# Kernel tuning notes

Hardware: AMD Instinct MI355X
Metric: run time of the kernel (lower is better)

Reference implementation:

```python
import jax, jax.numpy as jnp
import numpy as np
import math

# dims
B, T, HFEAT, E = 32, 8, 128, 128
NUM_CLS, NUM_GLOBAL = 4, 2
NSP = NUM_CLS + NUM_GLOBAL            # 6 special tokens
SCALES = (1, 4, 8)
WINDOW = 4
NHEAD = 8
DH = E // NHEAD                        # 16
NLAYERS = 2                            # blocks per scale = ceil(6/3)
NS = len(SCALES)
F = 512                                # dim_feedforward
ROPE_BASE = 100000.0
NEG = -1e9


def setup_inputs() -> dict:
    key = jax.random.key(0)
    ks = jax.random.split(key, 16)
    def rn(k, shape, s=0.02):
        return jax.random.normal(k, shape, jnp.float32) * s
    inp = {
        'embeddings': jax.random.normal(ks[0], (B, T, NSP + HFEAT, E), jnp.float32),
        'cls_tokens': rn(ks[1], (NUM_CLS, E)),
        'global_tokens': rn(ks[2], (NUM_GLOBAL, E)),
        'Wq': rn(ks[3], (NS, NLAYERS, E, E)),
        'bq': jnp.zeros((NS, NLAYERS, E), jnp.float32),
        'Wk': rn(ks[4], (NS, NLAYERS, E, E)),
        'bk': jnp.zeros((NS, NLAYERS, E), jnp.float32),
        'Wv': rn(ks[5], (NS, NLAYERS, E, E)),
        'bv': jnp.zeros((NS, NLAYERS, E), jnp.float32),
        'Wo': rn(ks[6], (NS, NLAYERS, E, E)),
        'bo': jnp.zeros((NS, NLAYERS, E), jnp.float32),
        'ln1_g': jnp.ones((NS, NLAYERS, E), jnp.float32),
        'ln1_b': jnp.zeros((NS, NLAYERS, E), jnp.float32),
        'ln2_g': jnp.ones((NS, NLAYERS, E), jnp.float32),
        'ln2_b': jnp.zeros((NS, NLAYERS, E), jnp.float32),
        'W1': rn(ks[7], (NS, NLAYERS, E, F)),
        'b1': jnp.zeros((NS, NLAYERS, F), jnp.float32),
        'W2': rn(ks[8], (NS, NLAYERS, F, E)),
        'b2': jnp.zeros((NS, NLAYERS, E), jnp.float32),
        'out_g': jnp.ones((E,), jnp.float32),
        'out_b': jnp.zeros((E,), jnp.float32),
    }
    return inp


def _layernorm(x, g, b, eps=1e-5):
    mu = x.mean(-1, keepdims=True)
    var = ((x - mu) ** 2).mean(-1, keepdims=True)
    return (x - mu) * jax.lax.rsqrt(var + eps) * g + b


def _rope(x):
    # x: (BT, L, H, DH); rotate-half RoPE over head dim
    L = x.shape[1]
    half = DH // 2
    inv = ROPE_BASE ** (-jnp.arange(half, dtype=jnp.float32) / half)
    ang = jnp.arange(L, dtype=jnp.float32)[:, None] * inv[None, :]   # (L, half)
    cos = jnp.cos(ang)[None, :, None, :]
    sin = jnp.sin(ang)[None, :, None, :]
    x1, x2 = x[..., :half], x[..., half:]
    return jnp.concatenate([x1 * cos - x2 * sin, x1 * sin + x2 * cos], axis=-1)


def _sparse_bias(L):
    # global(first NSP) rows/cols fully connected, others window +-WINDOW, diag allowed
    i = jnp.arange(L)
    allowed = (jnp.abs(i[:, None] - i[None, :]) <= WINDOW) | (i[:, None] < NSP) | (i[None, :] < NSP)
    return jnp.where(allowed, 0.0, NEG).astype(jnp.float32)  # (L, L) additive


def _encoder(x, s, Wq, bq, Wk, bk, Wv, bv, Wo, bo, ln1_g, ln1_b, ln2_g, ln2_b, W1, b1, W2, b2, bias):
    # x: (BT, L, E); pre-norm transformer encoder with RoPE attention
    BT, L, _ = x.shape
    for l in range(NLAYERS):
        h = _layernorm(x, ln1_g[s, l], ln1_b[s, l])
        q = (h @ Wq[s, l] + bq[s, l]).reshape(BT, L, NHEAD, DH)
        k = (h @ Wk[s, l] + bk[s, l]).reshape(BT, L, NHEAD, DH)
        v = (h @ Wv[s, l] + bv[s, l]).reshape(BT, L, NHEAD, DH)
        q, k = _rope(q), _rope(k)
        scores = jnp.einsum('blhd,bmhd->bhlm', q, k) / math.sqrt(DH) + bias[None, None]
        attn = jax.nn.softmax(scores, axis=-1)
        o = jnp.einsum('bhlm,bmhd->blhd', attn, v).reshape(BT, L, E)
        x = x + o @ Wo[s, l] + bo[s, l]
        h2 = _layernorm(x, ln2_g[s, l], ln2_b[s, l])
        x = x + jax.nn.gelu(h2 @ W1[s, l] + b1[s, l]) @ W2[s, l] + b2[s, l]
    return x


def reference(embeddings, cls_tokens, global_tokens, Wq, bq, Wk, bk, Wv, bv, Wo, bo,
              ln1_g, ln1_b, ln2_g, ln2_b, W1, b1, W2, b2, out_g, out_b):
    Bb, Tt, HC, Ee = embeddings.shape
    feats = embeddings[..., NSP:, :]                                 # (B,T,H,E)
    specials = jnp.broadcast_to(
        jnp.concatenate([cls_tokens, global_tokens], axis=0)[None, None],
        (Bb, Tt, NSP, Ee))
    cls_per_scale = []
    for s, g in enumerate(SCALES):
        H = feats.shape[2]
        K = H // g  # H divisible by all scales
        grouped = feats.reshape(Bb, Tt, K, g, Ee).mean(axis=3)       # contiguous mean grouping
        seq = jnp.concatenate([specials, grouped], axis=2)           # (B,T,L,E)
        L = NSP + K
        x = seq.reshape(Bb * Tt, L, Ee)
        bias = _sparse_bias(L)
        out = _encoder(x, s, Wq, bq, Wk, bk, Wv, bv, Wo, bo,
                       ln1_g, ln1_b, ln2_g, ln2_b, W1, b1, W2, b2, bias)
        cls_per_scale.append(out.reshape(Bb, Tt, L, Ee)[..., :NUM_CLS, :])
    cls_out = jnp.stack(cls_per_scale, axis=0).mean(axis=0)          # (B,T,num_cls,E)
    cls_out = _layernorm(cls_out, out_g, out_b)
    return cls_out.reshape(Bb, Tt, NUM_CLS * Ee)
```

## Files before the change

### kernel.cpp

```cpp
#include <hip/hip_runtime.h>
#include <hip/hip_bf16.h>

#define BT     256
#define EDIM   128
#define NSP    6
#define RT     49664
#define O1     34304
#define O2     44032
#define KSTR   20

typedef unsigned short u16;
typedef short s16x8 __attribute__((ext_vector_type(8)));
typedef float f32x4 __attribute__((ext_vector_type(4)));

__device__ __forceinline__ float u2f(u16 u){ union{unsigned i; float f;} v; v.i=((unsigned)u)<<16; return v.f; }
__device__ __forceinline__ u16 f2u(float f){
  union{float f; unsigned i;} v; v.f = f;
  unsigned r = v.i + 0x7FFF + ((v.i >> 16) & 1);
  return (u16)(r >> 16);
}
__device__ __forceinline__ float ldin(const void* p, size_t idx, int flag){
  return flag ? u2f(((const u16*)p)[idx]) : ((const float*)p)[idx];
}
__device__ __forceinline__ void unp8(uint4 v, float* f){
  f[0]=u2f((u16)(v.x)); f[1]=u2f((u16)(v.x>>16));
  f[2]=u2f((u16)(v.y)); f[3]=u2f((u16)(v.y>>16));
  f[4]=u2f((u16)(v.z)); f[5]=u2f((u16)(v.z>>16));
  f[6]=u2f((u16)(v.w)); f[7]=u2f((u16)(v.w>>16));
}

__device__ __forceinline__ void rowinfo(int row, int& s, int& r, int& L, int& g){
  if (row < O1){ s=0; r=row;    L=134; g=1; }
  else if (row < O2){ s=1; r=row-O1; L=38; g=4; }
  else { s=2; r=row-O2; L=22; g=8; }
}

__device__ __forceinline__ float gelu_f(float x){
  float u = x*(1.5957691216f + 0.0713548162f*x*x);
  return x * __builtin_amdgcn_rcpf(1.f + __expf(-u));
}

__global__ void detect_k(const void* ln1g, int* flagp){
  unsigned v = *(const unsigned*)ln1g;
  *flagp = (v == 0x3F803F80u) ? 1 : 0;
}

struct CArg { const void* src; unsigned dstoff; unsigned n; unsigned inblk; unsigned outblk; };
struct CArgs { CArg a[12]; };
__global__ __launch_bounds__(256) void conv_k(CArgs ca, u16* stage, const int* flagp){
  int i = blockIdx.y;
  int flag = *flagp;
  const CArg& c = ca.a[i];
  for (unsigned idx = blockIdx.x*256u + threadIdx.x; idx < c.n; idx += gridDim.x*256u){
    unsigned blk = idx / c.inblk, r = idx % c.inblk;
    float v = flag ? u2f(((const u16*)c.src)[idx]) : ((const float*)c.src)[idx];
    stage[c.dstoff + blk*c.outblk + r] = flag ? ((const u16*)c.src)[idx] : f2u(v);
  }
}

__global__ __launch_bounds__(256) void convw_k(const void* s0, const void* s1, const void* s2,
                                               u16* dst, int K, int N, int Nsrc, const int* flagp)
{
  int flag = *flagp;
  const void* srcs[3] = {s0, s1, s2};
  int total = 6 * K * N;
  for (int idx = blockIdx.x*256 + threadIdx.x; idx < total; idx += gridDim.x*256) {
    int blk = idx / (K*N);
    int rem = idx % (K*N);
    int j = rem & 7;
    int t = rem >> 3;
    int n = t % N;
    int ck = t / N;
    int k = ck*8 + j;
    int w = n / Nsrc;
    int nn = n - w*Nsrc;
    size_t sidx = (size_t)blk*K*Nsrc + (size_t)k*Nsrc + nn;
    dst[idx] = flag ? ((const u16*)srcs[w])[sidx] : f2u(((const float*)srcs[w])[sidx]);
  }
}

__global__ __launch_bounds__(128) void build_k(const void* __restrict__ emb,
                                               const void* __restrict__ cls,
                                               const void* __restrict__ glob,
                                               float* __restrict__ x,
                                               u16* __restrict__ H,
                                               const u16* __restrict__ lnG,
                                               const u16* __restrict__ lnB,
                                               const int* flagp)
{
  __shared__ float red[4];
  int flag = *flagp;
  int row = blockIdx.x, e = threadIdx.x;
  int s, r, L, g; rowinfo(row, s, r, L, g);
  int seq = r / L, pos = r % L;
  float val;
  if (pos < NSP) {
    val = (pos < 4) ? ldin(cls, pos*EDIM + e, flag) : ldin(glob, (pos-4)*EDIM + e, flag);
  } else {
    int k = pos - NSP;
    size_t base = ((size_t)seq*134 + NSP + (size_t)k*g)*EDIM + e;
    float sum = 0.f;
    for (int j = 0; j < g; j++) sum += ldin(emb, base + (size_t)j*EDIM, flag);
    val = sum / (float)g;
  }
  x[(size_t)row*EDIM + e] = val;
  int wid = e >> 6;
  float sum = val, ss = val*val;
  #pragma unroll
  for (int off = 32; off; off >>= 1) { sum += __shfl_xor(sum, off); ss += __shfl_xor(ss, off); }
  if ((e & 63) == 0) { red[wid] = sum; red[2+wid] = ss; }
  __syncthreads();
  float ts = red[0]+red[1], tss = red[2]+red[3];
  float mu = ts * (1.f/128.f);
  float var = tss * (1.f/128.f) - mu*mu;
  float rs = rsqrtf(var + 1e-5f);
  const u16* gp = lnG + s*2*EDIM;
  const u16* bp = lnB + s*2*EDIM;
  H[(size_t)row*EDIM + e] = f2u((val-mu)*rs*u2f(gp[e]) + u2f(bp[e]));
}

template<int EPI>
__global__ __launch_bounds__(256) void gemm64_k(
    const u16* __restrict__ A,
    const u16* __restrict__ Wt, const u16* __restrict__ Bias,
    u16* __restrict__ C, int ldc, int N, int layer,
    float* __restrict__ X, u16* __restrict__ H,
    const u16* __restrict__ lnG, const u16* __restrict__ lnB, int lnidx)
{
  __shared__ u16 As[4][16*136];
  __shared__ u16 Bs[16*128*8];
  const int row0 = blockIdx.x * 64;
  const int n0 = blockIdx.y * 128;
  const int s = row0 < O1 ? 0 : (row0 < O2 ? 1 : 2);
  const u16* Wp = Wt + (size_t)(s*2+layer)*128*N;
  const u16* bp = Bias + (size_t)(s*2+layer)*N + n0;
  const int tid = threadIdx.x;
  const int lane = tid & 63, w = tid >> 6;
  const int g = lane >> 4, l15 = lane & 15;

  #pragma unroll
  for (int i = 0; i < 4; i++) {
    int unit = lane + i*64;
    int r = unit >> 4, kc = unit & 15;
    *(uint4*)&As[w][r*136 + kc*8] = *(const uint4*)(A + (size_t)(row0 + w*16 + r)*128 + kc*8);
  }
  #pragma unroll
  for (int i = 0; i < 8; i++) {
    int u = tid + i*256;
    int kb = u >> 7, nn = u & 127;
    *(uint4*)&Bs[u*8] = *(const uint4*)(Wp + ((size_t)kb*N + n0 + nn)*8);
  }
  __syncthreads();

  f32x4 acc[8];
  #pragma unroll
  for (int nt = 0; nt < 8; nt++) acc[nt] = (f32x4){0.f,0.f,0.f,0.f};
  #pragma unroll
  for (int ks = 0; ks < 4; ks++) {
    int c = ks*4 + g;
    s16x8 af = *(const s16x8*)&As[w][l15*136 + c*8];
    #pragma unroll
    for (int nt = 0; nt < 8; nt++) {
      s16x8 bf = *(const s16x8*)&Bs[(c*128 + nt*16 + l15)*8];
      acc[nt] = __builtin_amdgcn_mfma_f32_16x16x32_bf16(af, bf, acc[nt], 0, 0, 0);
    }
  }

  float bb[8];
  #pragma unroll
  for (int nt = 0; nt < 8; nt++) bb[nt] = u2f(bp[nt*16 + l15]);

  if (EPI == 0) {
    #pragma unroll
    for (int reg = 0; reg < 4; reg++) {
      int row = row0 + w*16 + g*4 + reg;
      #pragma unroll
      for (int nt = 0; nt < 8; nt++)
        C[(size_t)row*ldc + n0 + nt*16 + l15] = f2u(acc[nt][reg] + bb[nt]);
    }
  } else {
    float gam[8], bet[8];
    const u16* gp = lnG + (s*2+lnidx)*EDIM;
    const u16* bpn = lnB + (s*2+lnidx)*EDIM;
    #pragma unroll
    for (int nt = 0; nt < 8; nt++) { gam[nt] = u2f(gp[nt*16+l15]); bet[nt] = u2f(bpn[nt*16+l15]); }
    #pragma unroll
    for (int reg = 0; reg < 4; reg++) {
      int row = row0 + w*16 + g*4 + reg;
      float vals[8], ps = 0.f, pss = 0.f;
      #pragma unroll
      for (int nt = 0; nt < 8; nt++) {
        size_t cidx = (size_t)row*128 + nt*16 + l15;
        float v = acc[nt][reg] + bb[nt] + X[cidx];
        vals[nt] = v; ps += v; pss += v*v;
      }
      #pragma unroll
      for (int off = 1; off < 16; off <<= 1) { ps += __shfl_xor(ps, off); pss += __shfl_xor(pss, off); }
      float mu = ps * (1.f/128.f);
      float var = pss * (1.f/128.f) - mu*mu;
      float rs = rsqrtf(var + 1e-5f);
      #pragma unroll
      for (int nt = 0; nt < 8; nt++) {
        size_t cidx = (size_t)row*128 + nt*16 + l15;
        X[cidx] = vals[nt];
        H[cidx] = f2u((vals[nt]-mu)*rs*gam[nt] + bet[nt]);
      }
    }
  }
}

template<int LNFUSE>
__global__ __launch_bounds__(256) void ffn_k(
    const u16* __restrict__ A,
    const u16* __restrict__ W1t, const u16* __restrict__ B1,
    const u16* __restrict__ W2t, const u16* __restrict__ B2,
    float* __restrict__ X,
    u16* __restrict__ H, const u16* __restrict__ lnG, const u16* __restrict__ lnB,
    int lnidx, int layer)
{
  __shared__ u16 Ts[4][16*40];
  const int row0 = blockIdx.x * 64;
  const int s = row0 < O1 ? 0 : (row0 < O2 ? 1 : 2);
  const u16* W1p = W1t + (size_t)(s*2+layer)*65536;
  const u16* b1p = B1 + (s*2+layer)*512;
  const u16* W2p = W2t + (size_t)(s*2+layer)*65536;
  const u16* b2p = B2 + (s*2+layer)*128;
  const int tid = threadIdx.x;
  const int lane = tid & 63, w = tid >> 6;
  const int g = lane >> 4, l15 = lane & 15;

  s16x8 af[4];
  {
    const u16* arow = A + (size_t)(row0 + w*16 + l15)*128;
    #pragma unroll
    for (int ks = 0; ks < 4; ks++) af[ks] = *(const s16x8*)(arow + (ks*4 + g)*8);
  }

  const u16* w1base = W1p + ((size_t)g*512 + l15)*8;
  const u16* w2base = W2p + ((size_t)g*128 + l15)*8;

  f32x4 acc2[8];
  #pragma unroll
  for (int nt = 0; nt < 8; nt++) acc2[nt] = (f32x4){0.f,0.f,0.f,0.f};

  s16x8 bw1[8];
  #pragma unroll
  for (int ks = 0; ks < 4; ks++) {
    #pragma unroll
    for (int nt = 0; nt < 2; nt++)
      bw1[ks*2+nt] = *(const s16x8*)(w1base + (size_t)(ks*2048 + nt*16)*8);
  }

  for (int f0 = 0; f0 < 512; f0 += 32) {
    s16x8 bw2[8];
    #pragma unroll
    for (int nt = 0; nt < 8; nt++)
      bw2[nt] = *(const s16x8*)(w2base + (size_t)(f0*16 + nt*16)*8);

    f32x4 acc1[2];
    acc1[0] = (f32x4){0.f,0.f,0.f,0.f};
    acc1[1] = (f32x4){0.f,0.f,0.f,0.f};
    #pragma unroll
    for (int ks = 0; ks < 4; ks++) {
      acc1[0] = __builtin_amdgcn_mfma_f32_16x16x32_bf16(af[ks], bw1[ks*2+0], acc1[0], 0, 0, 0);
      acc1[1] = __builtin_amdgcn_mfma_f32_16x16x32_bf16(af[ks], bw1[ks*2+1], acc1[1], 0, 0, 0);
    }

    {
      int fn = (f0 + 32) & 511;
      #pragma unroll
      for (int ks = 0; ks < 4; ks++) {
        #pragma unroll
        for (int nt = 0; nt < 2; nt++)
          bw1[ks*2+nt] = *(const s16x8*)(w1base + (size_t)(ks*2048 + fn + nt*16)*8);
      }
    }

    #pragma unroll
    for (int nt = 0; nt < 2; nt++) {
      float bb1 = u2f(b1p[f0 + nt*16 + l15]);
      #pragma unroll
      for (int reg = 0; reg < 4; reg++)
        Ts[w][(g*4+reg)*40 + nt*16 + l15] = f2u(gelu_f(acc1[nt][reg] + bb1));
    }

    s16x8 af2 = *(const s16x8*)&Ts[w][l15*40 + g*8];
    #pragma unroll
    for (int nt = 0; nt < 8; nt++)
      acc2[nt] = __builtin_amdgcn_mfma_f32_16x16x32_bf16(af2, bw2[nt], acc2[nt], 0, 0, 0);
  }

  float bb2[8];
  #pragma unroll
  for (int nt = 0; nt < 8; nt++) bb2[nt] = u2f(b2p[nt*16 + l15]);

  if (LNFUSE) {
    float gam[8], bet[8];
    const u16* gp = lnG + (s*2+lnidx)*EDIM;
    const u16* bpn = lnB + (s*2+lnidx)*EDIM;
    #pragma unroll
    for (int nt = 0; nt < 8; nt++) { gam[nt] = u2f(gp[nt*16+l15]); bet[nt] = u2f(bpn[nt*16+l15]); }
    #pragma unroll
    for (int reg = 0; reg < 4; reg++) {
      int row = row0 + w*16 + g*4 + reg;
      float vals[8], ps = 0.f, pss = 0.f;
      #pragma unroll
      for (int nt = 0; nt < 8; nt++) {
        size_t cidx = (size_t)row*128 + nt*16 + l15;
        float v = acc2[nt][reg] + bb2[nt] + X[cidx];
        vals[nt] = v; ps += v; pss += v*v;
      }
      #pragma unroll
      for (int off = 1; off < 16; off <<= 1) { ps += __shfl_xor(ps, off); pss += __shfl_xor(pss, off); }
      float mu = ps * (1.f/128.f);
      float var = pss * (1.f/128.f) - mu*mu;
      float rs = rsqrtf(var + 1e-5f);
      #pragma unroll
      for (int nt = 0; nt < 8; nt++) {
        size_t cidx = (size_t)row*128 + nt*16 + l15;
        X[cidx] = vals[nt];
        H[cidx] = f2u((vals[nt]-mu)*rs*gam[nt] + bet[nt]);
      }
    }
  } else {
    #pragma unroll
    for (int reg = 0; reg < 4; reg++) {
      int row = row0 + w*16 + g*4 + reg;
      #pragma unroll
      for (int nt = 0; nt < 8; nt++) {
        size_t cidx = (size_t)row*128 + nt*16 + l15;
        X[cidx] += acc2[nt][reg] + bb2[nt];
      }
    }
  }
}

__global__ __launch_bounds__(128) void attn_k(const u16* __restrict__ qkv, u16* __restrict__ o)
{
  __shared__ float Ks[134*KSTR];
  __shared__ float Vs[134*KSTR];
  int gseq = blockIdx.x, hd = blockIdx.y;
  int L, base;
  if (gseq < 256)      { L = 134; base = gseq*134; }
  else if (gseq < 512) { L = 38;  base = O1 + (gseq-256)*38; }
  else                 { L = 22;  base = O2 + (gseq-512)*22; }
  int tid = threadIdx.x;
  for (int u = tid; u < L*2; u += 128) {
    int kv = u & 1, row = u >> 1;
    const u16* p = qkv + (size_t)(base+row)*384 + 128 + kv*128 + hd*16;
    uint4 w0 = *(const uint4*)p, w1 = *(const uint4*)(p+8);
    float f[16];
    unp8(w0, f); unp8(w1, f+8);
    if (kv == 0) {
      #pragma unroll
      for (int d = 0; d < 8; d++) {
        float inv = __expf(-(float)d * (11.512925465f/8.f));
        float ang = (float)row * inv;
        float cs = __cosf(ang), sn = __sinf(ang);
        float a = f[d], b = f[d+8];
        f[d]   = a*cs - b*sn;
        f[d+8] = a*sn + b*cs;
      }
    }
    float* dst = (kv ? Vs : Ks) + row*KSTR;
    #pragma unroll
    for (int d = 0; d < 16; d++) dst[d] = f[d];
  }
  __syncthreads();

  for (int it = tid; it < L - NSP; it += 128) {
    int row = NSP + it;
    const u16* qp = qkv + (size_t)(base+row)*384 + hd*16;
    uint4 w0 = *(const uint4*)qp, w1 = *(const uint4*)(qp+8);
    float q[16]; unp8(w0, q); unp8(w1, q+8);
    #pragma unroll
    for (int d = 0; d < 8; d++) {
      float inv = __expf(-(float)d * (11.512925465f/8.f));
      float ang = (float)row * inv;
      float cs = __cosf(ang), sn = __sinf(ang);
      float a = q[d], b = q[d+8];
      q[d]   = a*cs - b*sn;
      q[d+8] = a*sn + b*cs;
    }
    float m = -1e30f, l = 0.f, oa[16] = {};
    auto step = [&](int j){
      const float4* kr = (const float4*)(Ks + j*KSTR);
      float4 k0 = kr[0], k1 = kr[1], k2 = kr[2], k3 = kr[3];
      float sc = q[0]*k0.x + q[1]*k0.y + q[2]*k0.z + q[3]*k0.w
               + q[4]*k1.x + q[5]*k1.y + q[6]*k1.z + q[7]*k1.w
               + q[8]*k2.x + q[9]*k2.y + q[10]*k2.z + q[11]*k2.w
               + q[12]*k3.x + q[13]*k3.y + q[14]*k3.z + q[15]*k3.w;
      sc *= 0.25f;
      float nm = fmaxf(m, sc);
      float scale = __expf(m - nm);
      float pexp = __expf(sc - nm);
      l = l*scale + pexp;
      const float4* vr = (const float4*)(Vs + j*KSTR);
      float4 v0 = vr[0], v1 = vr[1], v2 = vr[2], v3 = vr[3];
      oa[0]=oa[0]*scale+pexp*v0.x;  oa[1]=oa[1]*scale+pexp*v0.y;
      oa[2]=oa[2]*scale+pexp*v0.z;  oa[3]=oa[3]*scale+pexp*v0.w;
      oa[4]=oa[4]*scale+pexp*v1.x;  oa[5]=oa[5]*scale+pexp*v1.y;
      oa[6]=oa[6]*scale+pexp*v1.z;  oa[7]=oa[7]*scale+pexp*v1.w;
      oa[8]=oa[8]*scale+pexp*v2.x;  oa[9]=oa[9]*scale+pexp*v2.y;
      oa[10]=oa[10]*scale+pexp*v2.z; oa[11]=oa[11]*scale+pexp*v2.w;
      oa[12]=oa[12]*scale+pexp*v3.x; oa[13]=oa[13]*scale+pexp*v3.y;
      oa[14]=oa[14]*scale+pexp*v3.z; oa[15]=oa[15]*scale+pexp*v3.w;
      m = nm;
    };
    #pragma unroll
    for (int j = 0; j < NSP; j++) step(j);
    int jlo = (row-4 > NSP) ? row-4 : NSP;
    int jhi = (row+4 < L-1) ? row+4 : L-1;
    for (int j = jlo; j <= jhi; j++) step(j);
    float invl = 1.f/l;
    u16* op = o + (size_t)(base+row)*EDIM + hd*16;
    #pragma unroll
    for (int d = 0; d < 16; d++) op[d] = f2u(oa[d]*invl);
  }

  if (tid < 96) {
    int row = tid >> 4;
    int u = tid & 15;
    const u16* qp = qkv + (size_t)(base+row)*384 + hd*16;
    uint4 w0 = *(const uint4*)qp, w1 = *(const uint4*)(qp+8);
    float q[16]; unp8(w0, q); unp8(w1, q+8);
    #pragma unroll
    for (int d = 0; d < 8; d++) {
      float inv = __expf(-(float)d * (11.512925465f/8.f));
      float ang = (float)row * inv;
      float cs = __cosf(ang), sn = __sinf(ang);
      float a = q[d], b = q[d+8];
      q[d]   = a*cs - b*sn;
      q[d+8] = a*sn + b*cs;
    }
    float m = -1e30f, l = 0.f, oa[16] = {};
    for (int j = u; j < L; j += 16) {
      const float4* kr = (const float4*)(Ks + j*KSTR);
      float4 k0 = kr[0], k1 = kr[1], k2 = kr[2], k3 = kr[3];
      float sc = q[0]*k0.x + q[1]*k0.y + q[2]*k0.z + q[3]*k0.w
               + q[4]*k1.x + q[5]*k1.y + q[6]*k1.z + q[7]*k1.w
               + q[8]*k2.x + q[9]*k2.y + q[10]*k2.z + q[11]*k2.w
               + q[12]*k3.x + q[13]*k3.y + q[14]*k3.z + q[15]*k3.w;
      sc *= 0.25f;
      float nm = fmaxf(m, sc);
      float scale = __expf(m - nm);
      float pexp = __expf(sc - nm);
      l = l*scale + pexp;
      const float4* vr = (const float4*)(Vs + j*KSTR);
      float4 v0 = vr[0], v1 = vr[1], v2 = vr[2], v3 = vr[3];
      oa[0]=oa[0]*scale+pexp*v0.x;  oa[1]=oa[1]*scale+pexp*v0.y;
      oa[2]=oa[2]*scale+pexp*v0.z;  oa[3]=oa[3]*scale+pexp*v0.w;
      oa[4]=oa[4]*scale+pexp*v1.x;  oa[5]=oa[5]*scale+pexp*v1.y;
      oa[6]=oa[6]*scale+pexp*v1.z;  oa[7]=oa[7]*scale+pexp*v1.w;
      oa[8]=oa[8]*scale+pexp*v2.x;  oa[9]=oa[9]*scale+pexp*v2.y;
      oa[10]=oa[10]*scale+pexp*v2.z; oa[11]=oa[11]*scale+pexp*v2.w;
      oa[12]=oa[12]*scale+pexp*v3.x; oa[13]=oa[13]*scale+pexp*v3.y;
      oa[14]=oa[14]*scale+pexp*v3.z; oa[15]=oa[15]*scale+pexp*v3.w;
      m = nm;
    }
    #pragma unroll
    for (int off = 1; off < 16; off <<= 1) {
      float m2 = __shfl_xor(m, off);
      float l2 = __shfl_xor(l, off);
      float nm = fmaxf(m, m2);
      float s1 = __expf(m - nm), s2 = __expf(m2 - nm);
      #pragma unroll
      for (int d = 0; d < 16; d++) {
        float o2 = __shfl_xor(oa[d], off);
        oa[d] = oa[d]*s1 + o2*s2;
      }
      l = l*s1 + l2*s2;
      m = nm;
    }
    if (u == 0) {
      float invl = 1.f/l;
      u16* op = o + (size_t)(base+row)*EDIM + hd*16;
      #pragma unroll
      for (int d = 0; d < 16; d++) op[d] = f2u(oa[d]*invl);
    }
  }
}

__global__ __launch_bounds__(256) void final_k(const float* __restrict__ x,
                                               const u16* __restrict__ G,
                                               const u16* __restrict__ Bt,
                                               void* __restrict__ out, const int* flagp)
{
  int flag = *flagp;
  int wid = threadIdx.x >> 6, lane = threadIdx.x & 63;
  int idx = blockIdx.x*4 + wid;
  int seq = idx >> 2, c = idx & 3;
  size_t r0 = ((size_t)seq*134 + c)*EDIM;
  size_t r1 = ((size_t)O1 + (size_t)seq*38 + c)*EDIM;
  size_t r2 = ((size_t)O2 + (size_t)seq*22 + c)*EDIM;
  float v0 = (x[r0+lane]    + x[r1+lane]    + x[r2+lane])    * (1.f/3.f);
  float v1 = (x[r0+64+lane] + x[r1+64+lane] + x[r2+64+lane]) * (1.f/3.f);
  float sum = v0 + v1;
  #pragma unroll
  for (int off = 32; off; off >>= 1) sum += __shfl_xor(sum, off);
  float mu = sum * (1.f/128.f);
  float d0 = v0 - mu, d1 = v1 - mu;
  float var = d0*d0 + d1*d1;
  #pragma unroll
  for (int off = 32; off; off >>= 1) var += __shfl_xor(var, off);
  var *= (1.f/128.f);
  float rs = rsqrtf(var + 1e-5f);
  float o0 = d0*rs*u2f(G[lane])    + u2f(Bt[lane]);
  float o1 = d1*rs*u2f(G[64+lane]) + u2f(Bt[64+lane]);
  size_t oi0 = (size_t)seq*512 + c*128 + lane;
  if (flag) { ((u16*)out)[oi0] = f2u(o0); ((u16*)out)[oi0+64] = f2u(o1); }
  else      { ((float*)out)[oi0] = o0;    ((float*)out)[oi0+64] = o1; }
}

#define S_WQKV 0u
#define S_BQKV 294912u
#define S_WO   297216u
#define S_BO   395520u
#define S_W1   396288u
#define S_B1   789504u
#define S_W2   792576u
#define S_B2   1185792u
#define S_L1G  1186560u
#define S_L1B  1187328u
#define S_L2G  1188096u
#define S_L2B  1188864u
#define S_OG   1189632u
#define S_OB   1189760u

extern "C" void kernel_launch(void* const* d_in, const int* in_sizes, int n_in,
                              void* d_out, int out_size, void* d_ws, size_t ws_size,
                              hipStream_t stream) {
  char* wsb = (char*)d_ws;
  int*   flagp = (int*)wsb;
  u16*   stage = (u16*)(wsb + 64);
  float* x     = (float*)(wsb + (size_t)2379840);
  u16*   h     = (u16*)(wsb + (size_t)27807808);
  u16*   qkv   = (u16*)(wsb + (size_t)40521792);

  detect_k<<<1, 1, 0, stream>>>(d_in[11], flagp);

  CArgs ca;
  CArg list[12] = {
    { d_in[4],  S_BQKV,       768, 128, 384 },
    { d_in[6],  S_BQKV+128u,  768, 128, 384 },
    { d_in[8],  S_BQKV+256u,  768, 128, 384 },
    { d_in[10], S_BO,         768, 128, 128 },
    { d_in[16], S_B1,        3072, 512, 512 },
    { d_in[18], S_B2,         768, 128, 128 },
    { d_in[11], S_L1G,        768, 128, 128 },
    { d_in[12], S_L1B,        768, 128, 128 },
    { d_in[13], S_L2G,        768, 128, 128 },
    { d_in[14], S_L2B,        768, 128, 128 },
    { d_in[19], S_OG,         128, 128, 128 },
    { d_in[20], S_OB,         128, 128, 128 },
  };
  for (int i = 0; i < 12; i++) ca.a[i] = list[i];
  conv_k<<<dim3(4, 12), 256, 0, stream>>>(ca, stage, flagp);

  convw_k<<<256, 256, 0, stream>>>(d_in[3], d_in[5], d_in[7], stage+S_WQKV, 128, 384, 128, flagp);
  convw_k<<<128, 256, 0, stream>>>(d_in[9], d_in[9], d_in[9], stage+S_WO,   128, 128, 128, flagp);
  convw_k<<<256, 256, 0, stream>>>(d_in[15],d_in[15],d_in[15],stage+S_W1,   128, 512, 512, flagp);
  convw_k<<<256, 256, 0, stream>>>(d_in[17],d_in[17],d_in[17],stage+S_W2,   512, 128, 128, flagp);

  build_k<<<RT, 128, 0, stream>>>(d_in[0], d_in[1], d_in[2], x, h, stage+S_L1G, stage+S_L1B, flagp);

  for (int l = 0; l < 2; l++) {
    gemm64_k<0><<<dim3(RT/64, 3), 256, 0, stream>>>(h, stage+S_WQKV, stage+S_BQKV, qkv, 384, 384, l,
                                                    nullptr, nullptr, nullptr, nullptr, 0);
    attn_k<<<dim3(768, 8), 128, 0, stream>>>(qkv, h);
    gemm64_k<3><<<dim3(RT/64, 1), 256, 0, stream>>>(h, stage+S_WO, stage+S_BO, nullptr, 128, 128, l,
                                                    x, h, stage+S_L2G, stage+S_L2B, l);
    if (l == 0)
      ffn_k<1><<<RT/64, 256, 0, stream>>>(h, stage+S_W1, stage+S_B1, stage+S_W2, stage+S_B2, x, h, stage+S_L1G, stage+S_L1B, 1, l);
    else
      ffn_k<0><<<RT/64, 256, 0, stream>>>(h, stage+S_W1, stage+S_B1, stage+S_W2, stage+S_B2, x, nullptr, nullptr, nullptr, 0, l);
  }
  final_k<<<BT, 256, 0, stream>>>(x, stage+S_OG, stage+S_OB, d_out, flagp);
}
```

Measured before the change: 379.8 us.

## Fuse output projection, residual LayerNorm and FFN into one kernel with software pipelining

The Wo projection with its residual add and LN2 is merged into the FFN kernel. The normalized hidden state now stays in LDS and registers, and the residual lives in the accumulators, so the intermediate X/H global round trip and one launch per layer go away. The FFN loop is software-pipelined: the GELU tile is double-buffered in LDS and the W2 MMA for the previous chunk overlaps the W1 MMA for the current one. It also sets launch_bounds(256,3), which raises register pressure and may cost occupancy.

```diff
diff --git a/kernel.cpp b/kernel.cpp
--- a/kernel.cpp
+++ b/kernel.cpp
@@ -170,28 +170,206 @@
   #pragma unroll
   for (int nt = 0; nt < 8; nt++) bb[nt] = u2f(bp[nt*16 + l15]);
 
-  if (EPI == 0) {
-    #pragma unroll
-    for (int reg = 0; reg < 4; reg++) {
-      int row = row0 + w*16 + g*4 + reg;
-      #pragma unroll
-      for (int nt = 0; nt < 8; nt++)
-        C[(size_t)row*ldc + n0 + nt*16 + l15] = f2u(acc[nt][reg] + bb[nt]);
-    }
-  } else {
-    float gam[8], bet[8];
-    const u16* gp = lnG + (s*2+lnidx)*EDIM;
-    const u16* bpn = lnB + (s*2+lnidx)*EDIM;
-    #pragma unroll
-    for (int nt = 0; nt < 8; nt++) { gam[nt] = u2f(gp[nt*16+l15]); bet[nt] = u2f(bpn[nt*16+l15]); }
+  #pragma unroll
+  for (int reg = 0; reg < 4; reg++) {
+    int row = row0 + w*16 + g*4 + reg;
+    #pragma unroll
+    for (int nt = 0; nt < 8; nt++)
+      C[(size_t)row*ldc + n0 + nt*16 + l15] = f2u(acc[nt][reg] + bb[nt]);
+  }
+}
+
+template<int LNFUSE>
+__global__ __launch_bounds__(256, 3) void woffn_k(
+    const u16* __restrict__ A,
+    const u16* __restrict__ Wot, const u16* __restrict__ Bo,
+    const u16* __restrict__ W1t, const u16* __restrict__ B1,
+    const u16* __restrict__ W2t, const u16* __restrict__ B2,
+    float* __restrict__ X,
+    u16* __restrict__ H,
+    const u16* __restrict__ ln2G, const u16* __restrict__ ln2B,
+    const u16* __restrict__ ln1G, const u16* __restrict__ ln1B,
+    int layer)
+{
+  __shared__ u16 Hs[4][16*136];
+  __shared__ u16 Ts[2][4][16*40];
+  const int row0 = blockIdx.x * 64;
+  const int s = row0 < O1 ? 0 : (row0 < O2 ? 1 : 2);
+  const int sl = s*2 + layer;
+  const u16* Wop = Wot + (size_t)sl*16384;
+  const u16* bop = Bo  + sl*128;
+  const u16* W1p = W1t + (size_t)sl*65536;
+  const u16* b1p = B1  + sl*512;
+  const u16* W2p = W2t + (size_t)sl*65536;
+  const u16* b2p = B2  + sl*128;
+  const int tid = threadIdx.x;
+  const int lane = tid & 63, w = tid >> 6;
+  const int g = lane >> 4, l15 = lane & 15;
+
+  s16x8 af[4];
+  {
+    const u16* arow = A + (size_t)(row0 + w*16 + l15)*128;
+    #pragma unroll
+    for (int ks = 0; ks < 4; ks++) af[ks] = *(const s16x8*)(arow + (ks*4 + g)*8);
+  }
+  const u16* wobase = Wop + ((size_t)g*128 + l15)*8;
+
+  f32x4 acc2[8];
+  #pragma unroll
+  for (int nt = 0; nt < 8; nt++) acc2[nt] = (f32x4){0.f,0.f,0.f,0.f};
+  #pragma unroll
+  for (int ks = 0; ks < 4; ks++) {
+    s16x8 bw[8];
+    #pragma unroll
+    for (int nt = 0; nt < 8; nt++)
+      bw[nt] = *(const s16x8*)(wobase + ((size_t)ks*4096 + nt*128));
+    #pragma unroll
+    for (int nt = 0; nt < 8; nt++)
+      acc2[nt] = __builtin_amdgcn_mfma_f32_16x16x32_bf16(af[ks], bw[nt], acc2[nt], 0, 0, 0);
+  }
+
+  {
+    float gam[8], bet[8], bo_[8];
+    const u16* gp  = ln2G + sl*EDIM;
+    const u16* bp2 = ln2B + sl*EDIM;
+    #pragma unroll
+    for (int nt = 0; nt < 8; nt++) {
+      gam[nt] = u2f(gp[nt*16+l15]); bet[nt] = u2f(bp2[nt*16+l15]);
+      bo_[nt] = u2f(bop[nt*16+l15]);
+    }
     #pragma unroll
     for (int reg = 0; reg < 4; reg++) {
       int row = row0 + w*16 + g*4 + reg;
       float vals[8], ps = 0.f, pss = 0.f;
       #pragma unroll
       for (int nt = 0; nt < 8; nt++) {
-        size_t cidx = (size_t)row*128 + nt*16 + l15;
-        float v = acc[nt][reg] + bb[nt] + X[cidx];
+        float v = acc2[nt][reg] + bo_[nt] + X[(size_t)row*128 + nt*16 + l15];
+        vals[nt] = v; ps += v; pss += v*v;
+      }
+      #pragma unroll
+      for (int off = 1; off < 16; off <<= 1) { ps += __shfl_xor(ps, off); pss += __shfl_xor(pss, off); }
+      float mu = ps * (1.f/128.f);
+      float var = pss * (1.f/128.f) - mu*mu;
+      float rs = rsqrtf(var + 1e-5f);
+      #pragma unroll
+      for (int nt = 0; nt < 8; nt++) {
+        acc2[nt][reg] = vals[nt];
+        Hs[w][(g*4+reg)*136 + nt*16 + l15] = f2u((vals[nt]-mu)*rs*gam[nt] + bet[nt]);
+      }
+    }
+  }
+
+  s16x8 hf[4];
+  #pragma unroll
+  for (int ks = 0; ks < 4; ks++) hf[ks] = *(const s16x8*)&Hs[w][l15*136 + (ks*4+g)*8];
+
+  const u16* w1base = W1p + ((size_t)g*512 + l15)*8;
+  const u16* w2base = W2p + ((size_t)g*128 + l15)*8;
+
+  s16x8 bw1[8];
+  #pragma unroll
+  for (int ks = 0; ks < 4; ks++)
+    #pragma unroll
+    for (int nt = 0; nt < 2; nt++)
+      bw1[ks*2+nt] = *(const s16x8*)(w1base + (size_t)(ks*2048 + nt*16)*8);
+
+  {
+    f32x4 acc1[2];
+    acc1[0] = (f32x4){0.f,0.f,0.f,0.f};
+    acc1[1] = (f32x4){0.f,0.f,0.f,0.f};
+    #pragma unroll
+    for (int ks = 0; ks < 4; ks++) {
+      acc1[0] = __builtin_amdgcn_mfma_f32_16x16x32_bf16(hf[ks], bw1[ks*2+0], acc1[0], 0, 0, 0);
+      acc1[1] = __builtin_amdgcn_mfma_f32_16x16x32_bf16(hf[ks], bw1[ks*2+1], acc1[1], 0, 0, 0);
+    }
+    #pragma unroll
+    for (int ks = 0; ks < 4; ks++)
+      #pragma unroll
+      for (int nt = 0; nt < 2; nt++)
+        bw1[ks*2+nt] = *(const s16x8*)(w1base + (size_t)(ks*2048 + 32 + nt*16)*8);
+    #pragma unroll
+    for (int nt = 0; nt < 2; nt++) {
+      float bb1 = u2f(b1p[nt*16 + l15]);
+      #pragma unroll
+      for (int reg = 0; reg < 4; reg++)
+        Ts[0][w][(g*4+reg)*40 + nt*16 + l15] = f2u(gelu_f(acc1[nt][reg] + bb1));
+    }
+  }
+
+  for (int i = 1; i < 16; i++) {
+    const int f0 = i*32, fp = f0 - 32;
+    u16* tsC = &Ts[i & 1][w][0];
+    const u16* tsP = &Ts[(i & 1) ^ 1][w][0];
+
+    s16x8 bw2a[4];
+    #pragma unroll
+    for (int nt = 0; nt < 4; nt++)
+      bw2a[nt] = *(const s16x8*)(w2base + (size_t)(fp*16 + nt*16)*8);
+    s16x8 af2p = *(const s16x8*)(tsP + l15*40 + g*8);
+
+    f32x4 acc1[2];
+    acc1[0] = (f32x4){0.f,0.f,0.f,0.f};
+    acc1[1] = (f32x4){0.f,0.f,0.f,0.f};
+    #pragma unroll
+    for (int ks = 0; ks < 4; ks++) {
+      acc1[0] = __builtin_amdgcn_mfma_f32_16x16x32_bf16(hf[ks], bw1[ks*2+0], acc1[0], 0, 0, 0);
+      acc1[1] = __builtin_amdgcn_mfma_f32_16x16x32_bf16(hf[ks], bw1[ks*2+1], acc1[1], 0, 0, 0);
+    }
+    {
+      const int fn = (f0 + 32) & 511;
+      #pragma unroll
+      for (int ks = 0; ks < 4; ks++)
+        #pragma unroll
+        for (int nt = 0; nt < 2; nt++)
+          bw1[ks*2+nt] = *(const s16x8*)(w1base + (size_t)(ks*2048 + fn + nt*16)*8);
+    }
+    s16x8 bw2b[4];
+    #pragma unroll
+    for (int nt = 0; nt < 4; nt++)
+      bw2b[nt] = *(const s16x8*)(w2base + (size_t)(fp*16 + 64 + nt*16)*8);
+
+    #pragma unroll
+    for (int nt = 0; nt < 2; nt++) {
+      float bb1 = u2f(b1p[f0 + nt*16 + l15]);
+      #pragma unroll
+      for (int reg = 0; reg < 4; reg++)
+        tsC[(g*4+reg)*40 + nt*16 + l15] = f2u(gelu_f(acc1[nt][reg] + bb1));
+    }
+
+    #pragma unroll
+    for (int nt = 0; nt < 4; nt++)
+      acc2[nt] = __builtin_amdgcn_mfma_f32_16x16x32_bf16(af2p, bw2a[nt], acc2[nt], 0, 0, 0);
+    #pragma unroll
+    for (int nt = 0; nt < 4; nt++)
+      acc2[4+nt] = __builtin_amdgcn_mfma_f32_16x16x32_bf16(af2p, bw2b[nt], acc2[4+nt], 0, 0, 0);
+  }
+
+  {
+    s16x8 af2p = *(const s16x8*)&Ts[1][w][l15*40 + g*8];
+    #pragma unroll
+    for (int nt = 0; nt < 8; nt++) {
+      s16x8 b = *(const s16x8*)(w2base + (size_t)(480*16 + nt*16)*8);
+      acc2[nt] = __builtin_amdgcn_mfma_f32_16x16x32_bf16(af2p, b, acc2[nt], 0, 0, 0);
+    }
+  }
+
+  float bb2[8];
+  #pragma unroll
+  for (int nt = 0; nt < 8; nt++) bb2[nt] = u2f(b2p[nt*16 + l15]);
+
+  if (LNFUSE) {
+    float gam[8], bet[8];
+    const u16* gp  = ln1G + (s*2+1)*EDIM;
+    const u16* bpn = ln1B + (s*2+1)*EDIM;
+    #pragma unroll
+    for (int nt = 0; nt < 8; nt++) { gam[nt] = u2f(gp[nt*16+l15]); bet[nt] = u2f(bpn[nt*16+l15]); }
+    #pragma unroll
+    for (int reg = 0; reg < 4; reg++) {
+      int row = row0 + w*16 + g*4 + reg;
+      float vals[8], ps = 0.f, pss = 0.f;
+      #pragma unroll
+      for (int nt = 0; nt < 8; nt++) {
+        float v = acc2[nt][reg] + bb2[nt];
         vals[nt] = v; ps += v; pss += v*v;
       }
       #pragma unroll
@@ -206,130 +384,14 @@
         H[cidx] = f2u((vals[nt]-mu)*rs*gam[nt] + bet[nt]);
       }
     }
-  }
-}
-
-template<int LNFUSE>
-__global__ __launch_bounds__(256) void ffn_k(
-    const u16* __restrict__ A,
-    const u16* __restrict__ W1t, const u16* __restrict__ B1,
-    const u16* __restrict__ W2t, const u16* __restrict__ B2,
-    float* __restrict__ X,
-    u16* __restrict__ H, const u16* __restrict__ lnG, const u16* __restrict__ lnB,
-    int lnidx, int layer)
-{
-  __shared__ u16 Ts[4][16*40];
-  const int row0 = blockIdx.x * 64;
-  const int s = row0 < O1 ? 0 : (row0 < O2 ? 1 : 2);
-  const u16* W1p = W1t + (size_t)(s*2+layer)*65536;
-  const u16* b1p = B1 + (s*2+layer)*512;
-  const u16* W2p = W2t + (size_t)(s*2+layer)*65536;
-  const u16* b2p = B2 + (s*2+layer)*128;
-  const int tid = threadIdx.x;
-  const int lane = tid & 63, w = tid >> 6;
-  const int g = lane >> 4, l15 = lane & 15;
-
-  s16x8 af[4];
-  {
-    const u16* arow = A + (size_t)(row0 + w*16 + l15)*128;
-    #pragma unroll
-    for (int ks = 0; ks < 4; ks++) af[ks] = *(const s16x8*)(arow + (ks*4 + g)*8);
-  }
-
-  const u16* w1base = W1p + ((size_t)g*512 + l15)*8;
-  const u16* w2base = W2p + ((size_t)g*128 + l15)*8;
-
-  f32x4 acc2[8];
-  #pragma unroll
-  for (int nt = 0; nt < 8; nt++) acc2[nt] = (f32x4){0.f,0.f,0.f,0.f};
-
-  s16x8 bw1[8];
-  #pragma unroll
-  for (int ks = 0; ks < 4; ks++) {
-    #pragma unroll
-    for (int nt = 0; nt < 2; nt++)
-      bw1[ks*2+nt] = *(const s16x8*)(w1base + (size_t)(ks*2048 + nt*16)*8);
-  }
-
-  for (int f0 = 0; f0 < 512; f0 += 32) {
-    s16x8 bw2[8];
-    #pragma unroll
-    for (int nt = 0; nt < 8; nt++)
-      bw2[nt] = *(const s16x8*)(w2base + (size_t)(f0*16 + nt*16)*8);
-
-    f32x4 acc1[2];
-    acc1[0] = (f32x4){0.f,0.f,0.f,0.f};
-    acc1[1] = (f32x4){0.f,0.f,0.f,0.f};
-    #pragma unroll
-    for (int ks = 0; ks < 4; ks++) {
-      acc1[0] = __builtin_amdgcn_mfma_f32_16x16x32_bf16(af[ks], bw1[ks*2+0], acc1[0], 0, 0, 0);
-      acc1[1] = __builtin_amdgcn_mfma_f32_16x16x32_bf16(af[ks], bw1[ks*2+1], acc1[1], 0, 0, 0);
-    }
-
-    {
-      int fn = (f0 + 32) & 511;
-      #pragma unroll
-      for (int ks = 0; ks < 4; ks++) {
-        #pragma unroll
-        for (int nt = 0; nt < 2; nt++)
-          bw1[ks*2+nt] = *(const s16x8*)(w1base + (size_t)(ks*2048 + fn + nt*16)*8);
-      }
-    }
-
-    #pragma unroll
-    for (int nt = 0; nt < 2; nt++) {
-      float bb1 = u2f(b1p[f0 + nt*16 + l15]);
-      #pragma unroll
-      for (int reg = 0; reg < 4; reg++)
-        Ts[w][(g*4+reg)*40 + nt*16 + l15] = f2u(gelu_f(acc1[nt][reg] + bb1));
-    }
-
-    s16x8 af2 = *(const s16x8*)&Ts[w][l15*40 + g*8];
-    #pragma unroll
-    for (int nt = 0; nt < 8; nt++)
-      acc2[nt] = __builtin_amdgcn_mfma_f32_16x16x32_bf16(af2, bw2[nt], acc2[nt], 0, 0, 0);
-  }
-
-  float bb2[8];
-  #pragma unroll
-  for (int nt = 0; nt < 8; nt++) bb2[nt] = u2f(b2p[nt*16 + l15]);
-
-  if (LNFUSE) {
-    float gam[8], bet[8];
-    const u16* gp = lnG + (s*2+lnidx)*EDIM;
-    const u16* bpn = lnB + (s*2+lnidx)*EDIM;
-    #pragma unroll
-    for (int nt = 0; nt < 8; nt++) { gam[nt] = u2f(gp[nt*16+l15]); bet[nt] = u2f(bpn[nt*16+l15]); }
+  } else {
     #pragma unroll
     for (int reg = 0; reg < 4; reg++) {
       int row = row0 + w*16 + g*4 + reg;
-      float vals[8], ps = 0.f, pss = 0.f;
       #pragma unroll
       for (int nt = 0; nt < 8; nt++) {
         size_t cidx = (size_t)row*128 + nt*16 + l15;
-        float v = acc2[nt][reg] + bb2[nt] + X[cidx];
-        vals[nt] = v; ps += v; pss += v*v;
-      }
-      #pragma unroll
-      for (int off = 1; off < 16; off <<= 1) { ps += __shfl_xor(ps, off); pss += __shfl_xor(pss, off); }
-      float mu = ps * (1.f/128.f);
-      float var = pss * (1.f/128.f) - mu*mu;
-      float rs = rsqrtf(var + 1e-5f);
-      #pragma unroll
-      for (int nt = 0; nt < 8; nt++) {
-        size_t cidx = (size_t)row*128 + nt*16 + l15;
-        X[cidx] = vals[nt];
-        H[cidx] = f2u((vals[nt]-mu)*rs*gam[nt] + bet[nt]);
-      }
-    }
-  } else {
-    #pragma unroll
-    for (int reg = 0; reg < 4; reg++) {
-      int row = row0 + w*16 + g*4 + reg;
-      #pragma unroll
-      for (int nt = 0; nt < 8; nt++) {
-        size_t cidx = (size_t)row*128 + nt*16 + l15;
-        X[cidx] += acc2[nt][reg] + bb2[nt];
+        X[cidx] = acc2[nt][reg] + bb2[nt];
       }
     }
   }
@@ -568,12 +630,16 @@
     gemm64_k<0><<<dim3(RT/64, 3), 256, 0, stream>>>(h, stage+S_WQKV, stage+S_BQKV, qkv, 384, 384, l,
                                                     nullptr, nullptr, nullptr, nullptr, 0);
     attn_k<<<dim3(768, 8), 128, 0, stream>>>(qkv, h);
-    gemm64_k<3><<<dim3(RT/64, 1), 256, 0, stream>>>(h, stage+S_WO, stage+S_BO, nullptr, 128, 128, l,
-                                                    x, h, stage+S_L2G, stage+S_L2B, l);
     if (l == 0)
-      ffn_k<1><<<RT/64, 256, 0, stream>>>(h, stage+S_W1, stage+S_B1, stage+S_W2, stage+S_B2, x, h, stage+S_L1G, stage+S_L1B, 1, l);
+      woffn_k<1><<<RT/64, 256, 0, stream>>>(h, stage+S_WO, stage+S_BO,
+                                            stage+S_W1, stage+S_B1, stage+S_W2, stage+S_B2,
+                                            x, h, stage+S_L2G, stage+S_L2B,
+                                            stage+S_L1G, stage+S_L1B, 0);
     else
-      ffn_k<0><<<RT/64, 256, 0, stream>>>(h, stage+S_W1, stage+S_B1, stage+S_W2, stage+S_B2, x, nullptr, nullptr, nullptr, 0, l);
+      woffn_k<0><<<RT/64, 256, 0, stream>>>(h, stage+S_WO, stage+S_BO,
+                                            stage+S_W1, stage+S_B1, stage+S_W2, stage+S_B2,
+                                            x, nullptr, stage+S_L2G, stage+S_L2B,
+                                            stage+S_L1G, stage+S_L1B, 1);
   }
   final_k<<<BT, 256, 0, stream>>>(x, stage+S_OG, stage+S_OB, d_out, flagp);
 }
```

New measurement: 363.3 us. 4.4% less time.
